# Kernel optimization log

Hardware: AMD Instinct MI355X
Metric: run time of the kernel (lower is better)

The kernel has to match this reference:

```python
import jax, jax.numpy as jnp
import numpy as np

B, S, D, H = 4, 2048, 1024, 16
HD = D // H  # head size = 64

def setup_inputs() -> dict:
    key = jax.random.key(0)
    ks = jax.random.split(key, 9)
    s = 1.0 / np.sqrt(D)
    inp = {"x": jax.random.normal(ks[0], (B, S, D), dtype=jnp.float32)}
    for i, n in enumerate(["q", "k", "v", "o"]):
        inp[f"W{n}"] = jax.random.uniform(ks[1 + 2 * i], (D, D), minval=-s, maxval=s, dtype=jnp.float32)
        inp[f"b{n}"] = jax.random.uniform(ks[2 + 2 * i], (D,), minval=-s, maxval=s, dtype=jnp.float32)
    return inp

def reference(x, Wq, bq, Wk, bk, Wv, bv, Wo, bo):
    b, s, d = x.shape
    # project and split heads: [b, h, s, hd]
    def heads(y):
        return y.reshape(b, s, H, HD).transpose(0, 2, 1, 3)
    q = heads(x @ Wq.T + bq)
    k = heads(x @ Wk.T + bk)
    v = heads(x @ Wv.T + bv)
    scores = jnp.einsum('bhqd,bhkd->bhqk', q, k) / jnp.sqrt(jnp.float32(HD))
    attn = jax.nn.softmax(scores, axis=-1)
    ctx = jnp.einsum('bhqk,bhkd->bhqd', attn, v)
    ctx = ctx.transpose(0, 2, 1, 3).reshape(b, s, d)
    return ctx @ Wo.T + bo
```

## Files before the change

### kernel.cpp

```cpp
#include <hip/hip_runtime.h>
#include <hip/hip_bf16.h>

typedef __bf16 bf16;
typedef __bf16 bf16x8 __attribute__((ext_vector_type(8)));
typedef __bf16 bf16x4 __attribute__((ext_vector_type(4)));
typedef float f32x4 __attribute__((ext_vector_type(4)));
typedef float f32x16 __attribute__((ext_vector_type(16)));
typedef unsigned int u32;
typedef u32 u32x4 __attribute__((ext_vector_type(4)));

#define B_ 4
#define S_ 2048
#define D_ 1024
#define H_ 16
#define HD_ 64
#define LOG2E 1.4426950408889634f

static __device__ __forceinline__ f32x4 mfma16(bf16x8 a, bf16x8 b, f32x4 c) {
  return __builtin_amdgcn_mfma_f32_16x16x32_bf16(a, b, c, 0, 0, 0);
}
static __device__ __forceinline__ f32x16 mfma32(bf16x8 a, bf16x8 b, f32x16 c) {
  return __builtin_amdgcn_mfma_f32_32x32x16_bf16(a, b, c, 0, 0, 0);
}
static __device__ __forceinline__ void gload_lds16(const void* g, void* l) {
  __builtin_amdgcn_global_load_lds(
      (const __attribute__((address_space(1))) void*)g,
      (__attribute__((address_space(3))) void*)l, 16, 0, 0);
}
static __device__ __forceinline__ u32 pack2(float lo, float hi) {
  union { bf16 h[2]; u32 u; } un;
  un.h[0] = (bf16)lo; un.h[1] = (bf16)hi;
  return un.u;
}

__global__ void cvt_kernel(const float* __restrict__ in, bf16* __restrict__ out, int n4) {
  int i = blockIdx.x * blockDim.x + threadIdx.x;
  const int stride = gridDim.x * blockDim.x;
  for (; i < n4; i += stride) {
    float4 v = reinterpret_cast<const float4*>(in)[i];
    bf16x4 o;
    o[0] = (bf16)v.x; o[1] = (bf16)v.y; o[2] = (bf16)v.z; o[3] = (bf16)v.w;
    reinterpret_cast<bf16x4*>(out)[i] = o;
  }
}
__global__ void cvtw_kernel(const float* __restrict__ w0, const float* __restrict__ w1,
                            const float* __restrict__ w2, const float* __restrict__ w3,
                            bf16* __restrict__ o0, bf16* __restrict__ o1,
                            bf16* __restrict__ o2, bf16* __restrict__ o3, int n4) {
  const float* in = blockIdx.y == 0 ? w0 : blockIdx.y == 1 ? w1 : blockIdx.y == 2 ? w2 : w3;
  bf16* out = blockIdx.y == 0 ? o0 : blockIdx.y == 1 ? o1 : blockIdx.y == 2 ? o2 : o3;
  const int i = blockIdx.x * blockDim.x + threadIdx.x;
  float4 v = reinterpret_cast<const float4*>(in)[i];
  bf16x4 o;
  o[0] = (bf16)v.x; o[1] = (bf16)v.y; o[2] = (bf16)v.z; o[3] = (bf16)v.w;
  reinterpret_cast<bf16x4*>(out)[i] = o;
}

template<bool OUT_BF16, bool BIAS_ROW>
__global__ __launch_bounds__(256)
void gemm_bt(const bf16* __restrict__ A, const bf16* __restrict__ W,
             const float* __restrict__ bias, void* __restrict__ Cout,
             int M, int N, int K, float scale) {
  __shared__ bf16 Alds[128 * 32];
  __shared__ bf16 Blds[128 * 32];
  const int tid = threadIdx.x;
  const int wave = tid >> 6, lane = tid & 63;
  const int g = lane >> 4, r16 = lane & 15;
  const unsigned nwgx = gridDim.x;
  const unsigned nwg = nwgx * gridDim.y;
  unsigned lid = blockIdx.x + nwgx * blockIdx.y;
  unsigned swz = (lid & 7) * (nwg >> 3) + (lid >> 3);
  const int m0 = (int)(swz / nwgx) * 128, n0 = (int)(swz % nwgx) * 128;
  const int wm = (wave >> 1) * 64, wn = (wave & 1) * 64;

  f32x4 acc[4][4] = {};

  const int srow = (wave << 5) + (lane >> 2);
  const int scol = (lane & 3) << 3;
  const int nkt = K >> 5;

  for (int kt = 0; kt < nkt; ++kt) {
    __syncthreads();
    const int kb = kt << 5;
    gload_lds16(&A[(size_t)(m0 + srow) * K + kb + scol],      &Alds[(wave << 10)]);
    gload_lds16(&A[(size_t)(m0 + srow + 16) * K + kb + scol], &Alds[(wave << 10) + 512]);
    gload_lds16(&W[(size_t)(n0 + srow) * K + kb + scol],      &Blds[(wave << 10)]);
    gload_lds16(&W[(size_t)(n0 + srow + 16) * K + kb + scol], &Blds[(wave << 10) + 512]);
    __syncthreads();

    bf16x8 af[4], bf_[4];
#pragma unroll
    for (int i = 0; i < 4; ++i) {
      af[i]  = *reinterpret_cast<const bf16x8*>(&Alds[(wm + i * 16 + r16) * 32 + g * 8]);
      bf_[i] = *reinterpret_cast<const bf16x8*>(&Blds[(wn + i * 16 + r16) * 32 + g * 8]);
    }
#pragma unroll
    for (int i = 0; i < 4; ++i)
#pragma unroll
      for (int j = 0; j < 4; ++j)
        acc[i][j] = mfma16(af[i], bf_[j], acc[i][j]);
  }

#pragma unroll
  for (int i = 0; i < 4; ++i) {
#pragma unroll
    for (int j = 0; j < 4; ++j) {
      const int col = n0 + wn + j * 16 + r16;
      float bcol = BIAS_ROW ? 0.f : bias[col];
#pragma unroll
      for (int r = 0; r < 4; ++r) {
        const int row = m0 + wm + i * 16 + g * 4 + r;
        const float bv = BIAS_ROW ? bias[row] : bcol;
        const float v = (acc[i][j][r] + bv) * scale;
        if (OUT_BF16)
          reinterpret_cast<bf16*>(Cout)[(size_t)row * N + col] = (bf16)v;
        else
          reinterpret_cast<float*>(Cout)[(size_t)row * N + col] = v;
      }
    }
  }
}

__global__ __launch_bounds__(256)
void attn_kernel(const bf16* __restrict__ Q, const bf16* __restrict__ K,
                 const bf16* __restrict__ Vt, bf16* __restrict__ CTX) {
  const unsigned nwg = gridDim.x * gridDim.y;
  const unsigned lid = blockIdx.x + gridDim.x * blockIdx.y;
  const unsigned swzid = (lid & 7) * (nwg >> 3) + (lid >> 3);
  const int bh = (int)(swzid >> 4);
  const int q0 = (int)(swzid & 15) * 128;
  const int h = bh & (H_ - 1), b = bh >> 4;
  const int tid = threadIdx.x, wave = tid >> 6, lane = tid & 63;
  const int l32 = lane & 31, hi = lane >> 5;

  const bf16* Qb  = Q  + ((size_t)b * S_) * D_ + h * HD_;
  const bf16* Kb  = K  + ((size_t)b * S_) * D_ + h * HD_;
  const bf16* Vtb = Vt + (size_t)(h * HD_) * (B_ * S_) + b * S_;

  __shared__ __align__(16) char lds[32768];
  char* kb0 = lds;
  char* kb1 = lds + 8192;
  char* vb0 = lds + 16384;
  char* vb1 = lds + 24576;

  const int q = q0 + wave * 32 + l32;
  bf16x8 qf[4];
#pragma unroll
  for (int ks = 0; ks < 4; ++ks)
    qf[ks] = *reinterpret_cast<const bf16x8*>(&Qb[(size_t)q * D_ + ks * 16 + hi * 8]);

  f32x16 ctx0 = {}, ctx1 = {};
  float lrun = 0.f;

  const int krow0 = wave * 16 + (lane >> 3);
  const int xs = ((lane & 7) ^ (lane >> 3)) * 8;
  const int stoff = wave * 2048;
  const int swl = (l32 & 7) << 4;

  auto stage = [&](char* kd, char* vd, int kv0) {
    const size_t kg = (size_t)(kv0 + krow0) * D_ + xs;
    const size_t vg = (size_t)krow0 * (B_ * S_) + kv0 + xs;
    gload_lds16(Kb + kg,                   kd + stoff);
    gload_lds16(Kb + kg + 8 * D_,          kd + stoff + 1024);
    gload_lds16(Vtb + vg,                  vd + stoff);
    gload_lds16(Vtb + vg + 8 * (B_ * S_),  vd + stoff + 1024);
  };

  auto qkt = [&](f32x16& s0, f32x16& s1, const char* bK) {
    const f32x16 z = {};
    __builtin_amdgcn_s_setprio(1);
    {
      const int co = (hi * 16) ^ swl;
      bf16x8 kf0 = *reinterpret_cast<const bf16x8*>(bK + l32 * 128 + co);
      bf16x8 kf1 = *reinterpret_cast<const bf16x8*>(bK + (32 + l32) * 128 + co);
      s0 = mfma32(kf0, qf[0], z);
      s1 = mfma32(kf1, qf[0], z);
    }
#pragma unroll
    for (int ks = 1; ks < 4; ++ks) {
      const int co = (ks * 32 + hi * 16) ^ swl;
      bf16x8 kf0 = *reinterpret_cast<const bf16x8*>(bK + l32 * 128 + co);
      bf16x8 kf1 = *reinterpret_cast<const bf16x8*>(bK + (32 + l32) * 128 + co);
      s0 = mfma32(kf0, qf[ks], s0);
      s1 = mfma32(kf1, qf[ks], s1);
    }
    __builtin_amdgcn_s_setprio(0);
  };

  auto smpv = [&](const f32x16& s0, const f32x16& s1, const char* bV) {
    u32 w0[8], w1[8];
    float r0 = 0.f, r1 = 0.f;
#pragma unroll
    for (int a = 0; a < 4; ++a)
#pragma unroll
      for (int c = 0; c < 2; ++c) {
        const float e0 = __builtin_amdgcn_exp2f(s0[4 * a + 2 * c]);
        const float e1 = __builtin_amdgcn_exp2f(s0[4 * a + 2 * c + 1]);
        w0[2 * a + c] = pack2(e0, e1); r0 += e0 + e1;
        const float f0 = __builtin_amdgcn_exp2f(s1[4 * a + 2 * c]);
        const float f1 = __builtin_amdgcn_exp2f(s1[4 * a + 2 * c + 1]);
        w1[2 * a + c] = pack2(f0, f1); r1 += f0 + f1;
      }
    float rs = r0 + r1;
    rs += __shfl_xor(rs, 32);
    lrun += rs;
#pragma unroll
    for (int T = 0; T < 2; ++T) {
      const u32* w = T ? w1 : w0;
#pragma unroll
      for (int k1 = 0; k1 < 2; ++k1) {
        auto rA = __builtin_amdgcn_permlane32_swap((int)w[4 * k1 + 0], (int)w[4 * k1 + 2], false, false);
        auto rB = __builtin_amdgcn_permlane32_swap((int)w[4 * k1 + 1], (int)w[4 * k1 + 3], false, false);
        u32x4 fw;
        fw[0] = (u32)rA[0]; fw[1] = (u32)rB[0]; fw[2] = (u32)rA[1]; fw[3] = (u32)rB[1];
        const bf16x8 pa = __builtin_bit_cast(bf16x8, fw);
        const int ksp = T * 2 + k1;
        const int co = (ksp * 32 + hi * 16) ^ swl;
        bf16x8 vf0 = *reinterpret_cast<const bf16x8*>(bV + l32 * 128 + co);
        bf16x8 vf1 = *reinterpret_cast<const bf16x8*>(bV + (32 + l32) * 128 + co);
        __builtin_amdgcn_s_setprio(1);
        ctx0 = mfma32(pa, vf0, ctx0);
        ctx1 = mfma32(pa, vf1, ctx1);
        __builtin_amdgcn_s_setprio(0);
      }
    }
  };

  stage(kb0, vb0, 0);
  __syncthreads();

  for (int t = 0; t < 32; ++t) {
    const char* kc = (t & 1) ? kb1 : kb0;
    const char* vc = (t & 1) ? vb1 : vb0;
    if (t < 31) stage((t & 1) ? kb0 : kb1, (t & 1) ? vb0 : vb1, (t + 1) * 64);
    f32x16 s0, s1;
    qkt(s0, s1, kc);
    smpv(s0, s1, vc);
    __syncthreads();
  }

  char* Cw = lds + wave * 4096;
#pragma unroll
  for (int rg = 0; rg < 16; ++rg) {
    const int ql = (rg & 3) + 8 * (rg >> 2) + 4 * hi;
    const float inv = 1.0f / __shfl(lrun, ql);
    const int swq = (ql & 7) << 4;
    *reinterpret_cast<bf16*>(Cw + ql * 128 + ((l32 * 2) ^ swq)) = (bf16)(ctx0[rg] * inv);
    *reinterpret_cast<bf16*>(Cw + ql * 128 + ((64 + l32 * 2) ^ swq)) = (bf16)(ctx1[rg] * inv);
  }
  asm volatile("" ::: "memory");
#pragma unroll
  for (int i = 0; i < 4; ++i) {
    const int s = i * 64 + lane;
    const int row = s >> 3, cs = (s & 7) * 16;
    bf16x8 v = *reinterpret_cast<const bf16x8*>(Cw + row * 128 + (cs ^ ((row & 7) << 4)));
    *reinterpret_cast<bf16x8*>(
        &CTX[(size_t)(b * S_ + q0 + wave * 32 + row) * D_ + h * HD_ + cs / 2]) = v;
  }
}

extern "C" void kernel_launch(void* const* d_in, const int* in_sizes, int n_in,
                              void* d_out, int out_size, void* d_ws, size_t ws_size,
                              hipStream_t stream) {
  const float* x  = (const float*)d_in[0];
  const float* Wq = (const float*)d_in[1]; const float* bq = (const float*)d_in[2];
  const float* Wk = (const float*)d_in[3]; const float* bk = (const float*)d_in[4];
  const float* Wv = (const float*)d_in[5]; const float* bv = (const float*)d_in[6];
  const float* Wo = (const float*)d_in[7]; const float* bo = (const float*)d_in[8];

  char* ws = (char*)d_ws;
  const size_t MB = 1048576;
  bf16* xb  = (bf16*)(ws);
  bf16* wqb = (bf16*)(ws + 16 * MB);
  bf16* wkb = (bf16*)(ws + 18 * MB);
  bf16* wvb = (bf16*)(ws + 20 * MB);
  bf16* wob = (bf16*)(ws + 22 * MB);
  bf16* qb  = (bf16*)(ws + 24 * MB);
  bf16* kb  = (bf16*)(ws + 40 * MB);
  bf16* vtb = (bf16*)(ws + 56 * MB);
  bf16* ctx = (bf16*)(ws + 72 * MB);

  cvt_kernel<<<2048, 256, 0, stream>>>(x, xb, 2097152);
  cvtw_kernel<<<dim3(1024, 4), 256, 0, stream>>>(Wq, Wk, Wv, Wo, wqb, wkb, wvb, wob, 262144);

  dim3 gg(1024 / 128, 8192 / 128);
  gemm_bt<true,  false><<<gg, 256, 0, stream>>>(xb, wqb, bq, qb, 8192, 1024, 1024, 0.125f * LOG2E);
  gemm_bt<true,  false><<<gg, 256, 0, stream>>>(xb, wkb, bk, kb, 8192, 1024, 1024, 1.0f);
  dim3 gv(8192 / 128, 1024 / 128);
  gemm_bt<true,  true ><<<gv, 256, 0, stream>>>(wvb, xb, bv, vtb, 1024, 8192, 1024, 1.0f);

  attn_kernel<<<dim3(2048 / 128, B_ * H_), 256, 0, stream>>>(qb, kb, vtb, ctx);

  gemm_bt<false, false><<<gg, 256, 0, stream>>>(ctx, wob, bo, d_out, 8192, 1024, 1024, 1.0f);
}
```

Measured before the change: 233.6 us.

## Replace projection GEMMs with triple-buffered 256x128-tile kernel using swizzled LDS

Swaps the 128x128, K=32, single-buffered GEMM for a 512-thread kernel with 256x128 tiles and K=64 steps. LDS is triple-buffered, and vmcnt waits let global-to-LDS loads for step t+2 overlap MFMA work on step t. An XOR swizzle on LDS columns avoids bank conflicts, and s_setprio raises priority around the MFMA bursts. The 144KB LDS footprint means only one block fits per CU despite the launch bound asking for two, and the workgroup-order swizzle for L2 locality is dropped.

```diff
diff --git a/kernel.cpp b/kernel.cpp
--- a/kernel.cpp
+++ b/kernel.cpp
@@ -57,48 +57,72 @@
 }
 
 template<bool OUT_BF16, bool BIAS_ROW>
-__global__ __launch_bounds__(256)
-void gemm_bt(const bf16* __restrict__ A, const bf16* __restrict__ W,
-             const float* __restrict__ bias, void* __restrict__ Cout,
-             int M, int N, int K, float scale) {
-  __shared__ bf16 Alds[128 * 32];
-  __shared__ bf16 Blds[128 * 32];
+__global__ __launch_bounds__(512, 2)
+void gemm2(const bf16* __restrict__ A, const bf16* __restrict__ W,
+           const float* __restrict__ bias, void* __restrict__ Cout,
+           int M, int N, int K, float scale) {
+  __shared__ __align__(16) char lds[147456];
   const int tid = threadIdx.x;
-  const int wave = tid >> 6, lane = tid & 63;
+  const int wave = tid >> 6;
+  const int lane = tid & 63;
   const int g = lane >> 4, r16 = lane & 15;
-  const unsigned nwgx = gridDim.x;
-  const unsigned nwg = nwgx * gridDim.y;
-  unsigned lid = blockIdx.x + nwgx * blockIdx.y;
-  unsigned swz = (lid & 7) * (nwg >> 3) + (lid >> 3);
-  const int m0 = (int)(swz / nwgx) * 128, n0 = (int)(swz % nwgx) * 128;
+  const int m0 = blockIdx.y * 256, n0 = blockIdx.x * 128;
   const int wm = (wave >> 1) * 64, wn = (wave & 1) * 64;
 
   f32x4 acc[4][4] = {};
 
-  const int srow = (wave << 5) + (lane >> 2);
-  const int scol = (lane & 3) << 3;
-  const int nkt = K >> 5;
-
-  for (int kt = 0; kt < nkt; ++kt) {
-    __syncthreads();
-    const int kb = kt << 5;
-    gload_lds16(&A[(size_t)(m0 + srow) * K + kb + scol],      &Alds[(wave << 10)]);
-    gload_lds16(&A[(size_t)(m0 + srow + 16) * K + kb + scol], &Alds[(wave << 10) + 512]);
-    gload_lds16(&W[(size_t)(n0 + srow) * K + kb + scol],      &Blds[(wave << 10)]);
-    gload_lds16(&W[(size_t)(n0 + srow + 16) * K + kb + scol], &Blds[(wave << 10) + 512]);
-    __syncthreads();
-
-    bf16x8 af[4], bf_[4];
-#pragma unroll
-    for (int i = 0; i < 4; ++i) {
-      af[i]  = *reinterpret_cast<const bf16x8*>(&Alds[(wm + i * 16 + r16) * 32 + g * 8]);
-      bf_[i] = *reinterpret_cast<const bf16x8*>(&Blds[(wn + i * 16 + r16) * 32 + g * 8]);
-    }
-#pragma unroll
-    for (int i = 0; i < 4; ++i)
-#pragma unroll
-      for (int j = 0; j < 4; ++j)
-        acc[i][j] = mfma16(af[i], bf_[j], acc[i][j]);
+  const int srow = tid >> 3;
+  const int scol = ((tid & 7) ^ (srow & 7)) * 8;
+  const int wdst = wave * 1024;
+  const int nkt = K >> 6;
+
+  auto stage = [&](int bi, int t) {
+    char* buf = lds + bi * 49152;
+    const int kb = t << 6;
+#pragma unroll
+    for (int q = 0; q < 4; ++q)
+      gload_lds16(&A[(size_t)(m0 + q * 64 + srow) * K + kb + scol],
+                  buf + q * 8192 + wdst);
+#pragma unroll
+    for (int q = 0; q < 2; ++q)
+      gload_lds16(&W[(size_t)(n0 + q * 64 + srow) * K + kb + scol],
+                  buf + 32768 + q * 8192 + wdst);
+  };
+
+  stage(0, 0);
+  stage(1, 1);
+  int cur = 0;
+
+  for (int t = 0; t < nkt; ++t) {
+    if (t + 1 < nkt) asm volatile("s_waitcnt vmcnt(6)" ::: "memory");
+    else             asm volatile("s_waitcnt vmcnt(0)" ::: "memory");
+    __builtin_amdgcn_s_barrier();
+    int nx2 = cur + 2; if (nx2 >= 3) nx2 -= 3;
+    if (t + 2 < nkt) stage(nx2, t + 2);
+
+    const char* bufA = lds + cur * 49152;
+    const char* bufB = bufA + 32768;
+#pragma unroll
+    for (int kk = 0; kk < 2; ++kk) {
+      bf16x8 af[4], bfr[4];
+#pragma unroll
+      for (int i = 0; i < 4; ++i) {
+        const int ra = wm + i * 16 + r16;
+        af[i]  = *reinterpret_cast<const bf16x8*>(
+            bufA + ra * 128 + (((4 * kk + g) ^ (ra & 7)) * 16));
+        const int rb = wn + i * 16 + r16;
+        bfr[i] = *reinterpret_cast<const bf16x8*>(
+            bufB + rb * 128 + (((4 * kk + g) ^ (rb & 7)) * 16));
+      }
+      __builtin_amdgcn_s_setprio(1);
+#pragma unroll
+      for (int i = 0; i < 4; ++i)
+#pragma unroll
+        for (int j = 0; j < 4; ++j)
+          acc[i][j] = mfma16(af[i], bfr[j], acc[i][j]);
+      __builtin_amdgcn_s_setprio(0);
+    }
+    cur = (cur + 1 == 3) ? 0 : cur + 1;
   }
 
 #pragma unroll
@@ -283,13 +307,13 @@
   cvt_kernel<<<2048, 256, 0, stream>>>(x, xb, 2097152);
   cvtw_kernel<<<dim3(1024, 4), 256, 0, stream>>>(Wq, Wk, Wv, Wo, wqb, wkb, wvb, wob, 262144);
 
-  dim3 gg(1024 / 128, 8192 / 128);
-  gemm_bt<true,  false><<<gg, 256, 0, stream>>>(xb, wqb, bq, qb, 8192, 1024, 1024, 0.125f * LOG2E);
-  gemm_bt<true,  false><<<gg, 256, 0, stream>>>(xb, wkb, bk, kb, 8192, 1024, 1024, 1.0f);
-  dim3 gv(8192 / 128, 1024 / 128);
-  gemm_bt<true,  true ><<<gv, 256, 0, stream>>>(wvb, xb, bv, vtb, 1024, 8192, 1024, 1.0f);
+  dim3 gq(1024 / 128, 8192 / 256);
+  gemm2<true,  false><<<gq, 512, 0, stream>>>(xb, wqb, bq, qb, 8192, 1024, 1024, 0.125f * LOG2E);
+  gemm2<true,  false><<<gq, 512, 0, stream>>>(xb, wkb, bk, kb, 8192, 1024, 1024, 1.0f);
+  dim3 gv(8192 / 128, 1024 / 256);
+  gemm2<true,  true ><<<gv, 512, 0, stream>>>(wvb, xb, bv, vtb, 1024, 8192, 1024, 1.0f);
 
   attn_kernel<<<dim3(2048 / 128, B_ * H_), 256, 0, stream>>>(qb, kb, vtb, ctx);
 
-  gemm_bt<false, false><<<gg, 256, 0, stream>>>(ctx, wob, bo, d_out, 8192, 1024, 1024, 1.0f);
-}
+  gemm2<false, false><<<gq, 512, 0, stream>>>(ctx, wob, bo, d_out, 8192, 1024, 1024, 1.0f);
+}
```

Measured after the change: 214.1 us. 1.09x faster.
